# Kernel optimization log

Hardware: AMD Instinct MI355X
Metric: run time of the kernel (lower is better)

Reference implementation:

```python
import jax, jax.numpy as jnp
import numpy as np

D_MODEL = 768
N_HEADS = 12
D_K = D_MODEL // N_HEADS
BATCH = 1
SEQ = 4096


def setup_inputs() -> dict:
    key = jax.random.key(0)
    kx, kq, kk, kv, ko = jax.random.split(key, 5)
    s = 1.0 / np.sqrt(D_MODEL)
    return {
        "x": jax.random.normal(kx, (BATCH, SEQ, D_MODEL), dtype=jnp.float32),
        "wq": jax.random.normal(kq, (D_MODEL, D_MODEL), dtype=jnp.float32) * s,
        "wk": jax.random.normal(kk, (D_MODEL, D_MODEL), dtype=jnp.float32) * s,
        "wv": jax.random.normal(kv, (D_MODEL, D_MODEL), dtype=jnp.float32) * s,
        "wo": jax.random.normal(ko, (D_MODEL, D_MODEL), dtype=jnp.float32) * s,
    }


def reference(x, wq, wk, wv, wo):
    B, S, D = x.shape
    H, dk = N_HEADS, D_K
    # nn.Linear(x) = x @ W.T ; reshape to [B,H,S,dk]
    def proj(w):
        return (x @ w.T).reshape(B, S, H, dk).transpose(0, 2, 1, 3)
    q, k, v = proj(wq), proj(wk), proj(wv)
    scores = jnp.einsum('bhqd,bhkd->bhqk', q, k) / np.sqrt(dk).astype(np.float32)
    attn = jax.nn.softmax(scores, axis=-1)
    out = jnp.einsum('bhqk,bhkd->bhqd', attn, v)
    out = out.transpose(0, 2, 1, 3).reshape(B, S, D)
    return out @ wo.T
```

## Files before the change

### kernel.cpp

```cpp
#include <hip/hip_runtime.h>
#include <stdint.h>

#define SEQ 4096
#define DMODEL 768
#define NHEADS 12
#define DKH 64

typedef __attribute__((ext_vector_type(8))) short short8;
typedef __attribute__((ext_vector_type(4))) float floatx4;

__device__ __forceinline__ unsigned short f2bf(float f) {
    unsigned int u = __float_as_uint(f);
    u += 0x7fffu + ((u >> 16) & 1u);
    return (unsigned short)(u >> 16);
}

__device__ __forceinline__ float exp2fast(float x) {
    return __builtin_amdgcn_exp2f(x);
}

__device__ __forceinline__ unsigned int cvt_pk_bf16(float lo, float hi) {
    unsigned int r;
    asm("v_cvt_pk_bf16_f32 %0, %1, %2" : "=v"(r) : "v"(lo), "v"(hi));
    return r;
}

__device__ __forceinline__ int swz(int row, int colb) {
    return colb ^ ((row & 7) << 4);
}

__device__ __forceinline__ void async_copy16(void* lds, const void* g) {
    __builtin_amdgcn_global_load_lds(
        (const __attribute__((address_space(1))) void*)g,
        (__attribute__((address_space(3))) void*)lds,
        16, 0, 0);
}

__global__ __launch_bounds__(256) void castk(const float* __restrict__ src,
                                             unsigned short* __restrict__ dst,
                                             int n4) {
    int i = blockIdx.x * 256 + threadIdx.x;
    if (i >= n4) return;
    float4 v = ((const float4*)src)[i];
    ushort4 o;
    o.x = f2bf(v.x); o.y = f2bf(v.y); o.z = f2bf(v.z); o.w = f2bf(v.w);
    ((ushort4*)dst)[i] = o;
}

__global__ __launch_bounds__(256) void castw(const float* __restrict__ w0,
                                             const float* __restrict__ w1,
                                             const float* __restrict__ w2,
                                             const float* __restrict__ w3,
                                             unsigned short* __restrict__ dst) {
    int b = blockIdx.x;
    int wsel = b / 576;
    int i = (b % 576) * 256 + threadIdx.x;
    const float* src = (wsel == 0) ? w0 : (wsel == 1) ? w1 : (wsel == 2) ? w2 : w3;
    float4 v = ((const float4*)src)[i];
    ushort4 o;
    o.x = f2bf(v.x); o.y = f2bf(v.y); o.z = f2bf(v.z); o.w = f2bf(v.w);
    ((ushort4*)(dst + (size_t)wsel * 589824))[i] = o;
}

#define STAGE_G(bsel, kb)                                                              \
    do {                                                                               \
        char* As_ = smem + (bsel) * 24576;                                             \
        _Pragma("unroll") for (int ii = 0; ii < 4; ii++) {                             \
            int o = ii * 4096 + t * 16;                                                \
            int row = o >> 7, colb = o & 127;                                          \
            async_copy16(As_ + ii * 4096 + wid * 1024,                                 \
                         (const char*)A + ((size_t)(rowBase + row) * DMODEL + (kb)) * 2 \
                             + swz(row, colb));                                        \
        }                                                                              \
        _Pragma("unroll") for (int ii = 0; ii < 2; ii++) {                             \
            int o = ii * 4096 + t * 16;                                                \
            int row = o >> 7, colb = o & 127;                                          \
            async_copy16(As_ + 16384 + ii * 4096 + wid * 1024,                         \
                         (const char*)B + ((size_t)(colBase + row) * DMODEL + (kb)) * 2 \
                             + swz(row, colb));                                        \
        }                                                                              \
    } while (0)

#define GEMM_COMPUTE(As, Bs)                                                           \
    do {                                                                               \
        short8 a_[4][2], b_[2][2];                                                     \
        _Pragma("unroll") for (int m = 0; m < 4; m++)                                  \
            _Pragma("unroll") for (int kk = 0; kk < 2; kk++) {                         \
                int row = wr * 64 + m * 16 + lr;                                       \
                int colb = kk * 64 + lg * 16;                                          \
                a_[m][kk] = *(const short8*)((As) + row * 128 + swz(row, colb));       \
            }                                                                          \
        _Pragma("unroll") for (int n = 0; n < 2; n++)                                  \
            _Pragma("unroll") for (int kk = 0; kk < 2; kk++) {                         \
                int row = wc * 32 + n * 16 + lr;                                       \
                int colb = kk * 64 + lg * 16;                                          \
                b_[n][kk] = *(const short8*)((Bs) + row * 128 + swz(row, colb));       \
            }                                                                          \
        _Pragma("unroll") for (int m = 0; m < 4; m++)                                  \
            _Pragma("unroll") for (int n = 0; n < 2; n++)                              \
                _Pragma("unroll") for (int kk = 0; kk < 2; kk++)                       \
                    acc[m][n] = __builtin_amdgcn_mfma_f32_16x16x32_bf16(               \
                        a_[m][kk], b_[n][kk], acc[m][n], 0, 0, 0);                     \
    } while (0)

__global__ __launch_bounds__(256, 2)
void gemm_qkv(const unsigned short* __restrict__ A,
              const unsigned short* __restrict__ W,
              unsigned short* __restrict__ OutBase, float qscale) {
    __shared__ __align__(128) char smem[49152];

    const int t = threadIdx.x;
    const int wid = t >> 6, lane = t & 63;
    const int lr = lane & 15, lg = lane >> 4;
    const int wr = wid >> 1, wc = wid & 1;
    const int rowBase = blockIdx.x * 128;
    const int proj = blockIdx.y / 12;
    const int colBase = (blockIdx.y % 12) * 64;
    const unsigned short* B = W + (size_t)proj * 589824;

    const floatx4 zero4 = {0.f, 0.f, 0.f, 0.f};
    floatx4 acc[4][2];
#pragma unroll
    for (int m = 0; m < 4; m++)
#pragma unroll
        for (int n = 0; n < 2; n++) acc[m][n] = zero4;

    STAGE_G(0, 0);
    for (int i = 0; i < 12; ++i) {
        __builtin_amdgcn_s_barrier();
        __builtin_amdgcn_sched_barrier(0);
        if (i < 11) {
            STAGE_G((i + 1) & 1, (i + 1) * 64);
            asm volatile("s_waitcnt vmcnt(6)" ::: "memory");
        } else {
            asm volatile("s_waitcnt vmcnt(0)" ::: "memory");
        }
        __builtin_amdgcn_s_barrier();
        __builtin_amdgcn_sched_barrier(0);
        char* As = smem + (i & 1) * 24576;
        GEMM_COMPUTE(As, As + 16384);
    }

    if (proj < 2) {
        unsigned short* O = OutBase + (size_t)proj * 3145728;
        float scale = (proj == 0) ? qscale : 1.0f;
#pragma unroll
        for (int m = 0; m < 4; m++)
#pragma unroll
            for (int n = 0; n < 2; n++)
#pragma unroll
                for (int r = 0; r < 4; r++) {
                    int srow = rowBase + wr * 64 + m * 16 + lg * 4 + r;
                    int col = colBase + wc * 32 + n * 16 + lr;
                    int h = col >> 6, d = col & 63;
                    O[((size_t)h * SEQ + srow) * DKH + d] = f2bf(acc[m][n][r] * scale);
                }
    } else {
        unsigned short* O = OutBase + 6291456;
#pragma unroll
        for (int m = 0; m < 4; m++)
#pragma unroll
            for (int n = 0; n < 2; n++) {
                int srow0 = rowBase + wr * 64 + m * 16 + lg * 4;
                int z = srow0 & 31;
                int pos0 = (srow0 & ~31) + 8 * ((z >> 2) & 3) + 4 * (z >> 4);
                int col = colBase + wc * 32 + n * 16 + lr;
                ushort4 o4;
                o4.x = f2bf(acc[m][n][0]);
                o4.y = f2bf(acc[m][n][1]);
                o4.z = f2bf(acc[m][n][2]);
                o4.w = f2bf(acc[m][n][3]);
                *(ushort4*)(O + (size_t)col * SEQ + pos0) = o4;
            }
    }
}

__global__ __launch_bounds__(256, 2)
void gemm_o(const unsigned short* __restrict__ A,
            const unsigned short* __restrict__ B,
            float* __restrict__ Out) {
    __shared__ __align__(128) char smem[49152];

    const int t = threadIdx.x;
    const int wid = t >> 6, lane = t & 63;
    const int lr = lane & 15, lg = lane >> 4;
    const int wr = wid >> 1, wc = wid & 1;
    const int rowBase = blockIdx.x * 128;
    const int colBase = blockIdx.y * 64;

    const floatx4 zero4 = {0.f, 0.f, 0.f, 0.f};
    floatx4 acc[4][2];
#pragma unroll
    for (int m = 0; m < 4; m++)
#pragma unroll
        for (int n = 0; n < 2; n++) acc[m][n] = zero4;

    STAGE_G(0, 0);
    for (int i = 0; i < 12; ++i) {
        __builtin_amdgcn_s_barrier();
        __builtin_amdgcn_sched_barrier(0);
        if (i < 11) {
            STAGE_G((i + 1) & 1, (i + 1) * 64);
            asm volatile("s_waitcnt vmcnt(6)" ::: "memory");
        } else {
            asm volatile("s_waitcnt vmcnt(0)" ::: "memory");
        }
        __builtin_amdgcn_s_barrier();
        __builtin_amdgcn_sched_barrier(0);
        char* As = smem + (i & 1) * 24576;
        GEMM_COMPUTE(As, As + 16384);
    }

#pragma unroll
    for (int m = 0; m < 4; m++)
#pragma unroll
        for (int n = 0; n < 2; n++)
#pragma unroll
            for (int r = 0; r < 4; r++) {
                int srow = rowBase + wr * 64 + m * 16 + lg * 4 + r;
                int col = colBase + wc * 32 + n * 16 + lr;
                Out[(size_t)srow * DMODEL + col] = acc[m][n][r];
            }
}

#define STAGE_KA(bsel, kv0)                                                            \
    do {                                                                               \
        char* Kd_ = smem + (bsel) * 16384;                                             \
        _Pragma("unroll") for (int ii = 0; ii < 4; ii++) {                             \
            int o = ii * 4096 + t * 16;                                                \
            int row = o >> 7, colb = o & 127;                                          \
            async_copy16(Kd_ + ii * 4096 + wid * 1024,                                 \
                         (const char*)(Kp + headOff + (size_t)((kv0) + row) * DKH)     \
                             + swz(row, colb));                                        \
        }                                                                              \
    } while (0)

#define STAGE_VA(kv0)                                                                  \
    do {                                                                               \
        char* Vd_ = smem + 32768;                                                      \
        _Pragma("unroll") for (int ii = 0; ii < 4; ii++) {                             \
            int o = ii * 4096 + t * 16;                                                \
            int row = o >> 8, colb = o & 255;                                          \
            async_copy16(Vd_ + ii * 4096 + wid * 1024,                                 \
                         (const char*)(Vt + (size_t)(h * DKH + row) * SEQ + (kv0))     \
                             + swz(row, colb));                                        \
        }                                                                              \
    } while (0)

__global__ __launch_bounds__(256, 3)
void attn_k(const unsigned short* __restrict__ Q,
            const unsigned short* __restrict__ Kp,
            const unsigned short* __restrict__ Vt,
            unsigned short* __restrict__ AO) {
    __shared__ __align__(128) char smem[49152];

    const int t = threadIdx.x;
    const int wid = t >> 6, lane = t & 63;
    const int lr = lane & 15, lg = lane >> 4;

    int nid = (blockIdx.x & 7) * 96 + (blockIdx.x >> 3);
    const int h = nid >> 6, qb = nid & 63;
    const size_t headOff = (size_t)h * SEQ * DKH;

    const unsigned short* qptr = Q + headOff + (size_t)(qb * 64 + wid * 16 + lr) * DKH + lg * 8;
    short8 qf[2];
    qf[0] = *(const short8*)qptr;
    qf[1] = *(const short8*)(qptr + 32);

    const short8 ones8 = {(short)0x3F80, (short)0x3F80, (short)0x3F80, (short)0x3F80,
                          (short)0x3F80, (short)0x3F80, (short)0x3F80, (short)0x3F80};
    const floatx4 zero4 = {0.f, 0.f, 0.f, 0.f};
    float mrun = -3.0e38f;
    floatx4 acc[4];
    floatx4 acc_l = zero4;
#pragma unroll
    for (int f = 0; f < 4; f++) acc[f] = zero4;

    STAGE_KA(0, 0);

    for (int tt = 0; tt < 32; ++tt) {
        asm volatile("s_waitcnt vmcnt(0)" ::: "memory");
        __builtin_amdgcn_s_barrier();
        __builtin_amdgcn_sched_barrier(0);
        STAGE_VA(tt * 128);
        if (tt < 31) STAGE_KA((tt + 1) & 1, (tt + 1) * 128);
        __builtin_amdgcn_sched_barrier(0);

        char* Ks = smem + (tt & 1) * 16384;
        char* Vs = smem + 32768;

        floatx4 s[8];
#pragma unroll
        for (int ct = 0; ct < 8; ct++) s[ct] = zero4;
        __builtin_amdgcn_s_setprio(1);
#pragma unroll
        for (int ct = 0; ct < 8; ct++)
#pragma unroll
            for (int kk = 0; kk < 2; kk++) {
                int row = ct * 16 + lr;
                int colb = kk * 64 + lg * 16;
                short8 kf = *(const short8*)(Ks + row * 128 + swz(row, colb));
                s[ct] = __builtin_amdgcn_mfma_f32_16x16x32_bf16(kf, qf[kk], s[ct], 0, 0, 0);
            }
        __builtin_amdgcn_s_setprio(0);

        float cm[8];
#pragma unroll
        for (int ct = 0; ct < 8; ct++)
            cm[ct] = fmaxf(fmaxf(s[ct][0], s[ct][1]), fmaxf(s[ct][2], s[ct][3]));
        float mt = fmaxf(fmaxf(fmaxf(cm[0], cm[1]), fmaxf(cm[2], cm[3])),
                         fmaxf(fmaxf(cm[4], cm[5]), fmaxf(cm[6], cm[7])));
        mt = fmaxf(mt, __shfl_xor(mt, 16));
        mt = fmaxf(mt, __shfl_xor(mt, 32));
        if (!__all(mt <= mrun + 8.0f)) {
            float mnew = fmaxf(mrun, mt);
            float al = exp2fast(mrun - mnew);
#pragma unroll
            for (int f = 0; f < 4; f++)
#pragma unroll
                for (int r = 0; r < 4; r++) acc[f][r] *= al;
            acc_l[0] *= al;
            mrun = mnew;
        }
#pragma unroll
        for (int ct = 0; ct < 8; ct++)
#pragma unroll
            for (int r = 0; r < 4; r++) s[ct][r] = exp2fast(s[ct][r] - mrun);

        if (tt < 31) asm volatile("s_waitcnt vmcnt(4)" ::: "memory");
        else         asm volatile("s_waitcnt vmcnt(0)" ::: "memory");
        __builtin_amdgcn_s_barrier();
        __builtin_amdgcn_sched_barrier(0);

        __builtin_amdgcn_s_setprio(1);
#pragma unroll
        for (int kk = 0; kk < 4; kk++) {
            uint4 pw;
            pw.x = cvt_pk_bf16(s[2 * kk][0], s[2 * kk][1]);
            pw.y = cvt_pk_bf16(s[2 * kk][2], s[2 * kk][3]);
            pw.z = cvt_pk_bf16(s[2 * kk + 1][0], s[2 * kk + 1][1]);
            pw.w = cvt_pk_bf16(s[2 * kk + 1][2], s[2 * kk + 1][3]);
            short8 pf = *(const short8*)&pw;
#pragma unroll
            for (int f = 0; f < 4; f++) {
                int row = f * 16 + lr;
                int byteo = (row * 256 + kk * 64 + lg * 16) ^ ((row & 7) << 4);
                short8 vf = *(const short8*)(Vs + byteo);
                acc[f] = __builtin_amdgcn_mfma_f32_16x16x32_bf16(vf, pf, acc[f], 0, 0, 0);
            }
            acc_l = __builtin_amdgcn_mfma_f32_16x16x32_bf16(ones8, pf, acc_l, 0, 0, 0);
        }
        __builtin_amdgcn_s_setprio(0);
    }

    float inv = 1.0f / acc_l[0];
    int srow = qb * 64 + wid * 16 + lr;
#pragma unroll
    for (int f = 0; f < 4; f++) {
        ushort4 o4;
        o4.x = f2bf(acc[f][0] * inv);
        o4.y = f2bf(acc[f][1] * inv);
        o4.z = f2bf(acc[f][2] * inv);
        o4.w = f2bf(acc[f][3] * inv);
        int col = h * DKH + f * 16 + lg * 4;
        *(ushort4*)(AO + (size_t)srow * DMODEL + col) = o4;
    }
}

extern "C" void kernel_launch(void* const* d_in, const int* in_sizes, int n_in,
                              void* d_out, int out_size, void* d_ws, size_t ws_size,
                              hipStream_t stream) {
    const float* x  = (const float*)d_in[0];
    const float* wq = (const float*)d_in[1];
    const float* wk = (const float*)d_in[2];
    const float* wv = (const float*)d_in[3];
    const float* wo = (const float*)d_in[4];

    char* ws = (char*)d_ws;
    unsigned short* xb  = (unsigned short*)(ws + 0);
    unsigned short* wqb = (unsigned short*)(ws + 6291456);
    unsigned short* wob = (unsigned short*)(ws + 9830400);
    unsigned short* Qb  = (unsigned short*)(ws + 11010048);
    unsigned short* Kb  = (unsigned short*)(ws + 17301504);
    unsigned short* VTb = (unsigned short*)(ws + 23592960);
    unsigned short* AOb = (unsigned short*)(ws + 29884416);

    castk<<<3072, 256, 0, stream>>>(x, xb, 786432);
    castw<<<2304, 256, 0, stream>>>(wq, wk, wv, wo, wqb);

    gemm_qkv<<<dim3(32, 36), 256, 0, stream>>>(xb, wqb, Qb, 0.18033688f);

    attn_k<<<dim3(768), 256, 0, stream>>>(Qb, Kb, VTb, AOb);

    gemm_o<<<dim3(32, 12), 256, 0, stream>>>(AOb, wob, (float*)d_out);
}
```

Measured before the change: 118.5 us.

## Switch attention to 32x32x16 MFMA with two waves per block

Rewrites the attention kernel to use 32x32x16 bf16 MFMA tiles, with each of two waves handling 32 query rows instead of four waves of 16. The staging loops for K and V are rewritten for 128 threads, and V is laid out as two 64-column halves. The row-sum is now computed with explicit VALU reductions in place of the extra ones-vector MFMA, and the V-transpose store permutation in the QKV GEMM is changed to match the new fragment layout. The aim is fewer MFMA instructions and LDS reads per FLOP. The trade-offs are fewer waves per block for latency hiding, higher register pressure, and more copy instructions per thread.

```diff
diff --git a/kernel.cpp b/kernel.cpp
--- a/kernel.cpp
+++ b/kernel.cpp
@@ -8,6 +8,7 @@
 
 typedef __attribute__((ext_vector_type(8))) short short8;
 typedef __attribute__((ext_vector_type(4))) float floatx4;
+typedef __attribute__((ext_vector_type(16))) float floatx16;
 
 __device__ __forceinline__ unsigned short f2bf(float f) {
     unsigned int u = __float_as_uint(f);
@@ -162,8 +163,7 @@
 #pragma unroll
             for (int n = 0; n < 2; n++) {
                 int srow0 = rowBase + wr * 64 + m * 16 + lg * 4;
-                int z = srow0 & 31;
-                int pos0 = (srow0 & ~31) + 8 * ((z >> 2) & 3) + 4 * (z >> 4);
+                int pos0 = (srow0 & ~15) | ((srow0 & 4) << 1) | ((srow0 & 8) >> 1);
                 int col = colBase + wc * 32 + n * 16 + lr;
                 ushort4 o4;
                 o4.x = f2bf(acc[m][n][0]);
@@ -226,10 +226,10 @@
 #define STAGE_KA(bsel, kv0)                                                            \
     do {                                                                               \
         char* Kd_ = smem + (bsel) * 16384;                                             \
-        _Pragma("unroll") for (int ii = 0; ii < 4; ii++) {                             \
-            int o = ii * 4096 + t * 16;                                                \
+        _Pragma("unroll") for (int ii = 0; ii < 8; ii++) {                             \
+            int o = ii * 2048 + t * 16;                                                \
             int row = o >> 7, colb = o & 127;                                          \
-            async_copy16(Kd_ + ii * 4096 + wid * 1024,                                 \
+            async_copy16(Kd_ + ii * 2048 + wid * 1024,                                 \
                          (const char*)(Kp + headOff + (size_t)((kv0) + row) * DKH)     \
                              + swz(row, colb));                                        \
         }                                                                              \
@@ -238,16 +238,17 @@
 #define STAGE_VA(kv0)                                                                  \
     do {                                                                               \
         char* Vd_ = smem + 32768;                                                      \
-        _Pragma("unroll") for (int ii = 0; ii < 4; ii++) {                             \
-            int o = ii * 4096 + t * 16;                                                \
-            int row = o >> 8, colb = o & 255;                                          \
-            async_copy16(Vd_ + ii * 4096 + wid * 1024,                                 \
-                         (const char*)(Vt + (size_t)(h * DKH + row) * SEQ + (kv0))     \
-                             + swz(row, colb));                                        \
-        }                                                                              \
+        _Pragma("unroll") for (int hh = 0; hh < 2; hh++)                               \
+            _Pragma("unroll") for (int ii = 0; ii < 4; ii++) {                         \
+                int o = ii * 2048 + t * 16;                                            \
+                int row = o >> 7, colb = o & 127;                                      \
+                async_copy16(Vd_ + hh * 8192 + ii * 2048 + wid * 1024,                 \
+                             (const char*)(Vt + (size_t)(h * DKH + row) * SEQ          \
+                                           + (kv0) + hh * 64) + swz(row, colb));       \
+            }                                                                          \
     } while (0)
 
-__global__ __launch_bounds__(256, 3)
+__global__ __launch_bounds__(128, 2)
 void attn_k(const unsigned short* __restrict__ Q,
             const unsigned short* __restrict__ Kp,
             const unsigned short* __restrict__ Vt,
@@ -256,25 +257,22 @@
 
     const int t = threadIdx.x;
     const int wid = t >> 6, lane = t & 63;
-    const int lr = lane & 15, lg = lane >> 4;
+    const int q31 = lane & 31, hi = lane >> 5;
 
     int nid = (blockIdx.x & 7) * 96 + (blockIdx.x >> 3);
     const int h = nid >> 6, qb = nid & 63;
     const size_t headOff = (size_t)h * SEQ * DKH;
 
-    const unsigned short* qptr = Q + headOff + (size_t)(qb * 64 + wid * 16 + lr) * DKH + lg * 8;
-    short8 qf[2];
-    qf[0] = *(const short8*)qptr;
-    qf[1] = *(const short8*)(qptr + 32);
-
-    const short8 ones8 = {(short)0x3F80, (short)0x3F80, (short)0x3F80, (short)0x3F80,
-                          (short)0x3F80, (short)0x3F80, (short)0x3F80, (short)0x3F80};
-    const floatx4 zero4 = {0.f, 0.f, 0.f, 0.f};
-    float mrun = -3.0e38f;
-    floatx4 acc[4];
-    floatx4 acc_l = zero4;
-#pragma unroll
-    for (int f = 0; f < 4; f++) acc[f] = zero4;
+    const unsigned short* qptr =
+        Q + headOff + (size_t)(qb * 64 + wid * 32 + q31) * DKH + hi * 8;
+    short8 qf[4];
+#pragma unroll
+    for (int ks = 0; ks < 4; ks++) qf[ks] = *(const short8*)(qptr + ks * 16);
+
+    const floatx16 z16 = {0.f, 0.f, 0.f, 0.f, 0.f, 0.f, 0.f, 0.f,
+                          0.f, 0.f, 0.f, 0.f, 0.f, 0.f, 0.f, 0.f};
+    float mrun = -3.0e38f, lrun = 0.f;
+    floatx16 accO[2] = {z16, z16};
 
     STAGE_KA(0, 0);
 
@@ -286,85 +284,100 @@
         if (tt < 31) STAGE_KA((tt + 1) & 1, (tt + 1) * 128);
         __builtin_amdgcn_sched_barrier(0);
 
-        char* Ks = smem + (tt & 1) * 16384;
-        char* Vs = smem + 32768;
-
-        floatx4 s[8];
-#pragma unroll
-        for (int ct = 0; ct < 8; ct++) s[ct] = zero4;
+        const char* Ks = smem + (tt & 1) * 16384;
+        const char* Vs = smem + 32768;
+
+        floatx16 s[4] = {z16, z16, z16, z16};
         __builtin_amdgcn_s_setprio(1);
 #pragma unroll
-        for (int ct = 0; ct < 8; ct++)
-#pragma unroll
-            for (int kk = 0; kk < 2; kk++) {
-                int row = ct * 16 + lr;
-                int colb = kk * 64 + lg * 16;
-                short8 kf = *(const short8*)(Ks + row * 128 + swz(row, colb));
-                s[ct] = __builtin_amdgcn_mfma_f32_16x16x32_bf16(kf, qf[kk], s[ct], 0, 0, 0);
+        for (int kb = 0; kb < 4; kb++)
+#pragma unroll
+            for (int ks = 0; ks < 4; ks++) {
+                int row = kb * 32 + q31;
+                int byteo = (row * 128 + ks * 32 + hi * 16) ^ ((q31 & 7) << 4);
+                short8 kf = *(const short8*)(Ks + byteo);
+                s[kb] = __builtin_amdgcn_mfma_f32_32x32x16_bf16(kf, qf[ks], s[kb], 0, 0, 0);
             }
         __builtin_amdgcn_s_setprio(0);
 
-        float cm[8];
-#pragma unroll
-        for (int ct = 0; ct < 8; ct++)
-            cm[ct] = fmaxf(fmaxf(s[ct][0], s[ct][1]), fmaxf(s[ct][2], s[ct][3]));
-        float mt = fmaxf(fmaxf(fmaxf(cm[0], cm[1]), fmaxf(cm[2], cm[3])),
-                         fmaxf(fmaxf(cm[4], cm[5]), fmaxf(cm[6], cm[7])));
-        mt = fmaxf(mt, __shfl_xor(mt, 16));
+        float mk[4];
+#pragma unroll
+        for (int kb = 0; kb < 4; kb++) {
+            float a = fmaxf(fmaxf(s[kb][0], s[kb][1]), fmaxf(s[kb][2], s[kb][3]));
+            float b = fmaxf(fmaxf(s[kb][4], s[kb][5]), fmaxf(s[kb][6], s[kb][7]));
+            float c = fmaxf(fmaxf(s[kb][8], s[kb][9]), fmaxf(s[kb][10], s[kb][11]));
+            float d = fmaxf(fmaxf(s[kb][12], s[kb][13]), fmaxf(s[kb][14], s[kb][15]));
+            mk[kb] = fmaxf(fmaxf(a, b), fmaxf(c, d));
+        }
+        float mt = fmaxf(fmaxf(mk[0], mk[1]), fmaxf(mk[2], mk[3]));
         mt = fmaxf(mt, __shfl_xor(mt, 32));
         if (!__all(mt <= mrun + 8.0f)) {
             float mnew = fmaxf(mrun, mt);
             float al = exp2fast(mrun - mnew);
 #pragma unroll
-            for (int f = 0; f < 4; f++)
-#pragma unroll
-                for (int r = 0; r < 4; r++) acc[f][r] *= al;
-            acc_l[0] *= al;
+            for (int fb = 0; fb < 2; fb++)
+#pragma unroll
+                for (int j = 0; j < 16; j++) accO[fb][j] *= al;
+            lrun *= al;
             mrun = mnew;
         }
 #pragma unroll
-        for (int ct = 0; ct < 8; ct++)
-#pragma unroll
-            for (int r = 0; r < 4; r++) s[ct][r] = exp2fast(s[ct][r] - mrun);
-
-        if (tt < 31) asm volatile("s_waitcnt vmcnt(4)" ::: "memory");
+        for (int kb = 0; kb < 4; kb++)
+#pragma unroll
+            for (int j = 0; j < 16; j++) s[kb][j] = exp2fast(s[kb][j] - mrun);
+        float sum = 0.f;
+#pragma unroll
+        for (int kb = 0; kb < 4; kb++) {
+            float a = (s[kb][0] + s[kb][1]) + (s[kb][2] + s[kb][3]);
+            float b = (s[kb][4] + s[kb][5]) + (s[kb][6] + s[kb][7]);
+            float c = (s[kb][8] + s[kb][9]) + (s[kb][10] + s[kb][11]);
+            float d = (s[kb][12] + s[kb][13]) + (s[kb][14] + s[kb][15]);
+            sum += (a + b) + (c + d);
+        }
+        sum += __shfl_xor(sum, 32);
+        lrun += sum;
+
+        if (tt < 31) asm volatile("s_waitcnt vmcnt(8)" ::: "memory");
         else         asm volatile("s_waitcnt vmcnt(0)" ::: "memory");
         __builtin_amdgcn_s_barrier();
         __builtin_amdgcn_sched_barrier(0);
 
         __builtin_amdgcn_s_setprio(1);
 #pragma unroll
-        for (int kk = 0; kk < 4; kk++) {
+        for (int c = 0; c < 8; c++) {
+            const int kb = c >> 1, r0 = (c & 1) * 8;
             uint4 pw;
-            pw.x = cvt_pk_bf16(s[2 * kk][0], s[2 * kk][1]);
-            pw.y = cvt_pk_bf16(s[2 * kk][2], s[2 * kk][3]);
-            pw.z = cvt_pk_bf16(s[2 * kk + 1][0], s[2 * kk + 1][1]);
-            pw.w = cvt_pk_bf16(s[2 * kk + 1][2], s[2 * kk + 1][3]);
+            pw.x = cvt_pk_bf16(s[kb][r0 + 0], s[kb][r0 + 1]);
+            pw.y = cvt_pk_bf16(s[kb][r0 + 2], s[kb][r0 + 3]);
+            pw.z = cvt_pk_bf16(s[kb][r0 + 4], s[kb][r0 + 5]);
+            pw.w = cvt_pk_bf16(s[kb][r0 + 6], s[kb][r0 + 7]);
             short8 pf = *(const short8*)&pw;
 #pragma unroll
-            for (int f = 0; f < 4; f++) {
-                int row = f * 16 + lr;
-                int byteo = (row * 256 + kk * 64 + lg * 16) ^ ((row & 7) << 4);
+            for (int fb = 0; fb < 2; fb++) {
+                int row = fb * 32 + q31;
+                int byteo = ((c >> 2) * 8192 + row * 128 + (c & 3) * 32 + hi * 16)
+                            ^ ((q31 & 7) << 4);
                 short8 vf = *(const short8*)(Vs + byteo);
-                acc[f] = __builtin_amdgcn_mfma_f32_16x16x32_bf16(vf, pf, acc[f], 0, 0, 0);
+                accO[fb] = __builtin_amdgcn_mfma_f32_32x32x16_bf16(vf, pf, accO[fb], 0, 0, 0);
             }
-            acc_l = __builtin_amdgcn_mfma_f32_16x16x32_bf16(ones8, pf, acc_l, 0, 0, 0);
         }
         __builtin_amdgcn_s_setprio(0);
     }
 
-    float inv = 1.0f / acc_l[0];
-    int srow = qb * 64 + wid * 16 + lr;
-#pragma unroll
-    for (int f = 0; f < 4; f++) {
-        ushort4 o4;
-        o4.x = f2bf(acc[f][0] * inv);
-        o4.y = f2bf(acc[f][1] * inv);
-        o4.z = f2bf(acc[f][2] * inv);
-        o4.w = f2bf(acc[f][3] * inv);
-        int col = h * DKH + f * 16 + lg * 4;
-        *(ushort4*)(AO + (size_t)srow * DMODEL + col) = o4;
-    }
+    float inv = 1.0f / lrun;
+    int srow = qb * 64 + wid * 32 + q31;
+#pragma unroll
+    for (int fb = 0; fb < 2; fb++)
+#pragma unroll
+        for (int rq = 0; rq < 4; rq++) {
+            ushort4 o4;
+            o4.x = f2bf(accO[fb][4 * rq + 0] * inv);
+            o4.y = f2bf(accO[fb][4 * rq + 1] * inv);
+            o4.z = f2bf(accO[fb][4 * rq + 2] * inv);
+            o4.w = f2bf(accO[fb][4 * rq + 3] * inv);
+            int col = h * DKH + fb * 32 + rq * 8 + hi * 4;
+            *(ushort4*)(AO + (size_t)srow * DMODEL + col) = o4;
+        }
 }
 
 extern "C" void kernel_launch(void* const* d_in, const int* in_sizes, int n_in,
@@ -390,7 +403,7 @@
 
     gemm_qkv<<<dim3(32, 36), 256, 0, stream>>>(xb, wqb, Qb, 0.18033688f);
 
-    attn_k<<<dim3(768), 256, 0, stream>>>(Qb, Kb, VTb, AOb);
+    attn_k<<<dim3(768), 128, 0, stream>>>(Qb, Kb, VTb, AOb);
 
     gemm_o<<<dim3(32, 12), 256, 0, stream>>>(AOb, wob, (float*)d_out);
 }
```

After: 131.4 us. +10.9%, slower.
